# Kernel optimization log

Measured on AMD Instinct MI355X. Metric: run time of the kernel, lower is better.

## Reference

```python
import jax, jax.numpy as jnp
import numpy as np

H = 3  # hidden size (matches nn.LSTM(3, 3, ...))


def _lstm_dir(x, Wih, Whh, bih, bhh, reverse):
    """One direction of one LSTM layer. x: [B,T,D]; PyTorch gate order i,f,g,o."""
    B = x.shape[0]
    xT = jnp.swapaxes(x, 0, 1)  # [T,B,D]
    # Precompute input projection for all timesteps (memory-bound GEMM once).
    x_proj = jnp.einsum('tbd,gd->tbg', xT, Wih) + (bih + bhh)  # [T,B,4H]

    def step(carry, xp):
        h, c = carry
        gates = xp + h @ Whh.T  # [B,4H]
        i = jax.nn.sigmoid(gates[:, :H])
        f = jax.nn.sigmoid(gates[:, H:2 * H])
        g = jnp.tanh(gates[:, 2 * H:3 * H])
        o = jax.nn.sigmoid(gates[:, 3 * H:])
        c = f * c + i * g
        h = o * jnp.tanh(c)
        return (h, c), h

    init = (jnp.zeros((B, H), x.dtype), jnp.zeros((B, H), x.dtype))
    _, hs = jax.lax.scan(step, init, x_proj, reverse=reverse)
    return jnp.swapaxes(hs, 0, 1)  # [B,T,H], time-aligned with input


def setup_inputs() -> dict:
    key = jax.random.key(0)
    ks = jax.random.split(key, 20)
    B, T = 8192, 512
    k = 1.0 / np.sqrt(H)

    def u(kk, shape):
        return jax.random.uniform(kk, shape, jnp.float32, -k, k)

    inp = {"x": jax.random.normal(ks[0], (B, T, 3), jnp.float32)}
    # layer 0: input dim 3; layer 1: input dim 2*H = 6
    inp.update({
        "W_ih_l0": u(ks[1], (4 * H, 3)),  "W_hh_l0": u(ks[2], (4 * H, H)),
        "b_ih_l0": u(ks[3], (4 * H,)),    "b_hh_l0": u(ks[4], (4 * H,)),
        "W_ih_l0r": u(ks[5], (4 * H, 3)), "W_hh_l0r": u(ks[6], (4 * H, H)),
        "b_ih_l0r": u(ks[7], (4 * H,)),   "b_hh_l0r": u(ks[8], (4 * H,)),
        "W_ih_l1": u(ks[9], (4 * H, 2 * H)),  "W_hh_l1": u(ks[10], (4 * H, H)),
        "b_ih_l1": u(ks[11], (4 * H,)),       "b_hh_l1": u(ks[12], (4 * H,)),
        "W_ih_l1r": u(ks[13], (4 * H, 2 * H)),"W_hh_l1r": u(ks[14], (4 * H, H)),
        "b_ih_l1r": u(ks[15], (4 * H,)),      "b_hh_l1r": u(ks[16], (4 * H,)),
        "W_lin": u(ks[17], (1, 2 * H)),       "b_lin": u(ks[18], (1,)),
    })
    return inp


def reference(x, W_ih_l0, W_hh_l0, b_ih_l0, b_hh_l0,
              W_ih_l0r, W_hh_l0r, b_ih_l0r, b_hh_l0r,
              W_ih_l1, W_hh_l1, b_ih_l1, b_hh_l1,
              W_ih_l1r, W_hh_l1r, b_ih_l1r, b_hh_l1r,
              W_lin, b_lin):
    # layer 0 (bidirectional)
    y0 = jnp.concatenate([
        _lstm_dir(x, W_ih_l0, W_hh_l0, b_ih_l0, b_hh_l0, False),
        _lstm_dir(x, W_ih_l0r, W_hh_l0r, b_ih_l0r, b_hh_l0r, True),
    ], axis=-1)  # [B,T,6]
    # layer 1 (bidirectional)
    y1 = jnp.concatenate([
        _lstm_dir(y0, W_ih_l1, W_hh_l1, b_ih_l1, b_hh_l1, False),
        _lstm_dir(y0, W_ih_l1r, W_hh_l1r, b_ih_l1r, b_hh_l1r, True),
    ], axis=-1)  # [B,T,6]
    last = y1[:, -1, :]  # [B,6]  (output sequence at final timestep)
    out = last @ W_lin.T + b_lin  # [B,1]
    return jax.nn.sigmoid(out.reshape(-1))  # [B]
```

## Files before the change

kernel.cpp:

```cpp
#include <hip/hip_runtime.h>


#define B_ 8192
#define T_ 512
#define LOG2E 1.4426950408889634f

typedef float v2f __attribute__((ext_vector_type(2)));

__device__ __forceinline__ float rcp_(float x)  { return __builtin_amdgcn_rcpf(x); }
__device__ __forceinline__ float exp2_(float x) { return __builtin_amdgcn_exp2f(x); }
__device__ __forceinline__ float sigm_(float x) {
  return rcp_(1.0f + exp2_(-LOG2E * x));
}
__device__ __forceinline__ float tanh_(float x) {
  return 1.0f - 2.0f * rcp_(1.0f + exp2_(2.0f * LOG2E * x));
}
__device__ __forceinline__ float act_(float p) { return rcp_(1.f + exp2_(p)); }

__device__ __forceinline__ v2f sp(float s) { return (v2f){s, s}; }
__device__ __forceinline__ v2f pkfma(v2f a, float b, v2f c) {
  return __builtin_elementwise_fma(a, sp(b), c);
}

template <int CTRL>
__device__ __forceinline__ float dppf(float v) {
  int s = __float_as_int(v);
  return __int_as_float(__builtin_amdgcn_update_dpp(s, s, CTRL, 0xF, 0xF, false));
}
#define QP0 dppf<0x00>
#define QP1 dppf<0x55>
#define QP2 dppf<0xAA>
#define QP3 dppf<0xFF>
#define SHL4 0x104
#define SHR4 0x114


template <bool DIRB>
__device__ __forceinline__ void l0_run(
    const float* __restrict__ x,
    const float* __restrict__ Wi, const float* __restrict__ Wh,
    const float* __restrict__ bi, const float* __restrict__ bh,
    float* __restrict__ yout, int b, int jl)
{
  const int jj = (jl < 3) ? jl : 0;
  const int ri = jj, rf = 3 + jj, rg = 6 + jj, ro = 9 + jj;
  const float sL = -LOG2E, sG = -2.f * LOG2E;

  float wi_i0 = Wi[ri*3+0]*sL, wi_i1 = Wi[ri*3+1]*sL, wi_i2 = Wi[ri*3+2]*sL;
  float wi_f0 = Wi[rf*3+0]*sL, wi_f1 = Wi[rf*3+1]*sL, wi_f2 = Wi[rf*3+2]*sL;
  float wi_g0 = Wi[rg*3+0]*sG, wi_g1 = Wi[rg*3+1]*sG, wi_g2 = Wi[rg*3+2]*sG;
  float wi_o0 = Wi[ro*3+0]*sL, wi_o1 = Wi[ro*3+1]*sL, wi_o2 = Wi[ro*3+2]*sL;
  float wh_i0 = Wh[ri*3+0]*sL, wh_i1 = Wh[ri*3+1]*sL, wh_i2 = Wh[ri*3+2]*sL;
  float wh_f0 = Wh[rf*3+0]*sL, wh_f1 = Wh[rf*3+1]*sL, wh_f2 = Wh[rf*3+2]*sL;
  float wh_g0 = Wh[rg*3+0]*sG, wh_g1 = Wh[rg*3+1]*sG, wh_g2 = Wh[rg*3+2]*sG;
  float wh_o0 = Wh[ro*3+0]*sL, wh_o1 = Wh[ro*3+1]*sL, wh_o2 = Wh[ro*3+2]*sL;
  float b_i = (bi[ri]+bh[ri])*sL, b_f = (bi[rf]+bh[rf])*sL;
  float b_g = (bi[rg]+bh[rg])*sG, b_o = (bi[ro]+bh[ro])*sL;

  float h = 0.f, c = 0.f, ha0 = 0.f, ha1 = 0.f, ha2 = 0.f;
  float hs0, hs1, hs2, hs3, hs4, hs5, hs6, hs7;

  const float*  xrow = x + (size_t)b * (T_ * 3);
  const float4* xq4  = (const float4*)xrow;
  const float2* xq2  = (const float2*)(xrow);
  float* ybase = yout + (size_t)b * (T_ * 3) + jj * 8;

  float4 pA; float2 pB; float4 qA; float2 qB;

#define LDQ(blk, A_, B_) do {                                             \
    A_ = xq4[(blk) * 6 + jl];                                             \
    B_ = xq2[(blk) * 12 + 8 + jl];                                        \
    __builtin_amdgcn_sched_barrier(0); } while (0)

#define STEPS(X0, X1, X2, HOUT) do {                                      \
    float _x0 = (X0), _x1 = (X1), _x2 = (X2);                             \
    float _pi = __builtin_fmaf(wi_i0, _x0, b_i);                          \
    _pi = __builtin_fmaf(wi_i1, _x1, _pi);                                \
    _pi = __builtin_fmaf(wi_i2, _x2, _pi);                                \
    float _qi = wh_i0 * ha0;                                              \
    _qi = __builtin_fmaf(wh_i1, ha1, _qi);                                \
    _qi = __builtin_fmaf(wh_i2, ha2, _qi);                                \
    float _pf = __builtin_fmaf(wi_f0, _x0, b_f);                          \
    _pf = __builtin_fmaf(wi_f1, _x1, _pf);                                \
    _pf = __builtin_fmaf(wi_f2, _x2, _pf);                                \
    float _qf = wh_f0 * ha0;                                              \
    _qf = __builtin_fmaf(wh_f1, ha1, _qf);                                \
    _qf = __builtin_fmaf(wh_f2, ha2, _qf);                                \
    float _pg = __builtin_fmaf(wi_g0, _x0, b_g);                          \
    _pg = __builtin_fmaf(wi_g1, _x1, _pg);                                \
    _pg = __builtin_fmaf(wi_g2, _x2, _pg);                                \
    float _qg = wh_g0 * ha0;                                              \
    _qg = __builtin_fmaf(wh_g1, ha1, _qg);                                \
    _qg = __builtin_fmaf(wh_g2, ha2, _qg);                                \
    float _po = __builtin_fmaf(wi_o0, _x0, b_o);                          \
    _po = __builtin_fmaf(wi_o1, _x1, _po);                                \
    _po = __builtin_fmaf(wi_o2, _x2, _po);                                \
    float _qo = wh_o0 * ha0;                                              \
    _qo = __builtin_fmaf(wh_o1, ha1, _qo);                                \
    _qo = __builtin_fmaf(wh_o2, ha2, _qo);                                \
    float _ig = act_(_pi + _qi);                                          \
    float _fg = act_(_pf + _qf);                                          \
    float _gg = __builtin_fmaf(2.f, act_(_pg + _qg), -1.f);               \
    float _og = act_(_po + _qo);                                          \
    c = __builtin_fmaf(_fg, c, _ig * _gg);                                \
    float _th = __builtin_fmaf(                                           \
        2.f, rcp_(1.f + exp2_(-2.f * LOG2E * c)), -1.f);                  \
    h = _og * _th;                                                        \
    ha0 = QP0(h); ha1 = QP1(h); ha2 = QP2(h);                             \
    HOUT = h; } while (0)

#define S0(A_, B_) STEPS(QP0(A_.x), QP0(A_.y), QP0(A_.z), hs0)
#define S1(A_, B_) STEPS(QP0(A_.w), QP1(A_.x), QP1(A_.y), hs1)
#define S2(A_, B_) STEPS(QP1(A_.z), QP1(A_.w), QP2(A_.x), hs2)
#define S3(A_, B_) STEPS(QP2(A_.y), QP2(A_.z), QP2(A_.w), hs3)
#define S4(A_, B_) STEPS(QP3(A_.x), QP3(A_.y), QP3(A_.z), hs4)
#define S5(A_, B_) STEPS(QP3(A_.w), QP0(B_.x), QP0(B_.y), hs5)
#define S6(A_, B_) STEPS(QP1(B_.x), QP1(B_.y), QP2(B_.x), hs6)
#define S7(A_, B_) STEPS(QP2(B_.y), QP3(B_.x), QP3(B_.y), hs7)

#define PROCQ(A_, B_) do {                                                \
    if (DIRB) { S7(A_,B_); S6(A_,B_); S5(A_,B_); S4(A_,B_);               \
                S3(A_,B_); S2(A_,B_); S1(A_,B_); S0(A_,B_); }             \
    else      { S0(A_,B_); S1(A_,B_); S2(A_,B_); S3(A_,B_);               \
                S4(A_,B_); S5(A_,B_); S6(A_,B_); S7(A_,B_); } } while (0)

#define STQ(blk) do {                                                     \
    if (jl < 3) {                                                         \
      float4* _o = (float4*)(ybase + (blk) * 24);                         \
      _o[0] = make_float4(hs0, hs1, hs2, hs3);                            \
      _o[1] = make_float4(hs4, hs5, hs6, hs7);                            \
    } } while (0)

#define BLK(k) (DIRB ? (63 - (k)) : (k))

  LDQ(BLK(0), pA, pB);
  LDQ(BLK(1), qA, qB);
  for (int k = 0; k < 64; k += 2) {
    PROCQ(pA, pB);
    STQ(BLK(k));
    if (k + 2 < 64) LDQ(BLK(k + 2), pA, pB);
    PROCQ(qA, qB);
    STQ(BLK(k + 1));
    if (k + 3 < 64) LDQ(BLK(k + 3), qA, qB);
  }
#undef LDQ
#undef STEPS
#undef S0
#undef S1
#undef S2
#undef S3
#undef S4
#undef S5
#undef S6
#undef S7
#undef PROCQ
#undef STQ
#undef BLK
}

__global__ __launch_bounds__(256, 2) void lstm_l0_scalar(
    const float* __restrict__ x,
    const float* __restrict__ Wf_ih, const float* __restrict__ Wf_hh,
    const float* __restrict__ bf_ih, const float* __restrict__ bf_hh,
    const float* __restrict__ Wr_ih, const float* __restrict__ Wr_hh,
    const float* __restrict__ br_ih, const float* __restrict__ br_hh,
    float* __restrict__ y0f, float* __restrict__ y0b)
{
  int gid = blockIdx.x * 256 + threadIdx.x;
  const int nfwd = B_ * 4;
  if (gid < nfwd) {
    int b = gid >> 2, jl = gid & 3;
    l0_run<false>(x, Wf_ih, Wf_hh, bf_ih, bf_hh, y0f, b, jl);
  } else {
    int g2 = gid - nfwd;
    int b = g2 >> 2, jl = g2 & 3;
    l0_run<true>(x, Wr_ih, Wr_hh, br_ih, br_hh, y0b, b, jl);
  }
}

#define CELL_TAIL(HOUT)                                                   \
    float r0v = act_(pv.x);                                               \
    float ayv = act_(pv.y);                                               \
    float axv = __builtin_fmaf(avx, r0v, dvx);                            \
    float slx = dppf<SHL4>(axv), sly = dppf<SHL4>(ayv);                   \
    float srx = dppf<SHR4>(axv), sry = dppf<SHR4>(ayv);                   \
    float pig = axv * (qgo ? srx : slx);                                  \
    float gf  = qgo ? sry : ayv;                                          \
    float gO  = qgo ? ayv : sly;                                          \
    c = __builtin_fmaf(gf, c, pig);                                       \
    float th = __builtin_fmaf(                                            \
        2.f, rcp_(1.f + exp2_(-2.f * LOG2E * c)), -1.f);                  \
    h = gO * th;                                                          \
    ha0 = QP0(h); ha1 = QP1(h); ha2 = QP2(h);                             \
    HOUT = h;

__global__ __launch_bounds__(256, 1) void lstm_l1_fwd(
    const float* __restrict__ Wih1, const float* __restrict__ Whh1,
    const float* __restrict__ bih1, const float* __restrict__ bhh1,
    const float* __restrict__ Wih1r,
    const float* __restrict__ bih1r, const float* __restrict__ bhh1r,
    const float* __restrict__ Wlin, const float* __restrict__ blin,
    const float* __restrict__ y0f, const float* __restrict__ y0b,
    float* __restrict__ out)
{
  int tid  = blockIdx.x * 256 + threadIdx.x;
  int b    = tid >> 3;
  int lane = tid & 7;
  bool qgo = (lane & 4) != 0;
  int j = lane & 3; int jj = (j < 3) ? j : 0;
  const int ra = (qgo ? 6 : 0) + jj, rb = ra + 3;
  const float kx = qgo ? (-2.f * LOG2E) : (-LOG2E);
  const float ky = -LOG2E;
  const float avx = qgo ? 2.f : 1.f;
  const float dvx = qgo ? -1.f : 0.f;

  v2f w0 = {Wih1[ra*6+0]*kx, Wih1[rb*6+0]*ky},
      w1 = {Wih1[ra*6+1]*kx, Wih1[rb*6+1]*ky},
      w2 = {Wih1[ra*6+2]*kx, Wih1[rb*6+2]*ky},
      w3 = {Wih1[ra*6+3]*kx, Wih1[rb*6+3]*ky},
      w4 = {Wih1[ra*6+4]*kx, Wih1[rb*6+4]*ky},
      w5 = {Wih1[ra*6+5]*kx, Wih1[rb*6+5]*ky};
  v2f u0 = {Whh1[ra*3+0]*kx, Whh1[rb*3+0]*ky},
      u1 = {Whh1[ra*3+1]*kx, Whh1[rb*3+1]*ky},
      u2 = {Whh1[ra*3+2]*kx, Whh1[rb*3+2]*ky};
  v2f b2 = {(bih1[ra]+bhh1[ra])*kx, (bih1[rb]+bhh1[rb])*ky};

  const float4* yfq = (const float4*)(y0f + (size_t)b * (T_ * 3));
  const float4* ybq = (const float4*)(y0b + (size_t)b * (T_ * 3));

  const float* ufp = y0f + (size_t)b * (T_ * 3) + 63 * 24 + 7;
  const float* ubp = y0b + (size_t)b * (T_ * 3) + 63 * 24 + 7;
  float uf0 = ufp[0], uf1 = ufp[8], uf2 = ufp[16];
  float ub0 = ubp[0], ub1 = ubp[8], ub2 = ubp[16];

  float h = 0.f, c = 0.f, ha0 = 0.f, ha1 = 0.f, ha2 = 0.f;
  float hs0, hs1, hs2, hs3, hs4, hs5, hs6, hs7;
  float4 pf0, pf1, pf2, pf3, pf4, pf5, pb0, pb1, pb2, pb3, pb4, pb5;
  float4 qf0, qf1, qf2, qf3, qf4, qf5, qb0, qb1, qb2, qb3, qb4, qb5;

#define LDB(blk, F0,F1,F2,F3,F4,F5, G0,G1,G2,G3,G4,G5) do {               \
    const float4* _f = yfq + (blk) * 6;                                   \
    const float4* _g = ybq + (blk) * 6;                                   \
    F0 = _f[0]; F1 = _f[1]; F2 = _f[2];                                   \
    F3 = _f[3]; F4 = _f[4]; F5 = _f[5];                                   \
    G0 = _g[0]; G1 = _g[1]; G2 = _g[2];                                   \
    G3 = _g[3]; G4 = _g[4]; G5 = _g[5];                                   \
    __builtin_amdgcn_sched_barrier(0); } while (0)

#define STEPB(f0, f1, f2, g0, g1, g2, HOUT) do {                          \
    v2f pv = pkfma(w0, (f0), b2); pv = pkfma(w1, (f1), pv);               \
    pv = pkfma(w2, (f2), pv);                                             \
    v2f nv = w3 * sp(g0); nv = pkfma(w4, (g1), nv);                       \
    nv = pkfma(w5, (g2), nv);                                             \
    v2f uv = u0 * sp(ha0); uv = pkfma(u1, ha1, uv);                       \
    uv = pkfma(u2, ha2, uv);                                              \
    pv = (pv + nv) + uv;                                                  \
    CELL_TAIL(HOUT) } while (0)

#define PROCB(F0,F1,F2,F3,F4,F5, G0,G1,G2,G3,G4,G5) do {                  \
    STEPB(F0.x, F2.x, F4.x,  G0.x, G2.x, G4.x, hs0);                      \
    STEPB(F0.y, F2.y, F4.y,  G0.y, G2.y, G4.y, hs1);                      \
    STEPB(F0.z, F2.z, F4.z,  G0.z, G2.z, G4.z, hs2);                      \
    STEPB(F0.w, F2.w, F4.w,  G0.w, G2.w, G4.w, hs3);                      \
    STEPB(F1.x, F3.x, F5.x,  G1.x, G3.x, G5.x, hs4);                      \
    STEPB(F1.y, F3.y, F5.y,  G1.y, G3.y, G5.y, hs5);                      \
    STEPB(F1.z, F3.z, F5.z,  G1.z, G3.z, G5.z, hs6);                      \
    STEPB(F1.w, F3.w, F5.w,  G1.w, G3.w, G5.w, hs7); } while (0)

  LDB(0, pf0,pf1,pf2,pf3,pf4,pf5, pb0,pb1,pb2,pb3,pb4,pb5);
  LDB(1, qf0,qf1,qf2,qf3,qf4,qf5, qb0,qb1,qb2,qb3,qb4,qb5);
  for (int it = 0; it < 32; ++it) {
    PROCB(pf0,pf1,pf2,pf3,pf4,pf5, pb0,pb1,pb2,pb3,pb4,pb5);
    if (it < 31) LDB(2*it+2, pf0,pf1,pf2,pf3,pf4,pf5, pb0,pb1,pb2,pb3,pb4,pb5);
    PROCB(qf0,qf1,qf2,qf3,qf4,qf5, qb0,qb1,qb2,qb3,qb4,qb5);
    if (it < 31) LDB(2*it+3, qf0,qf1,qf2,qf3,qf4,qf5, qb0,qb1,qb2,qb3,qb4,qb5);
  }
  (void)hs0; (void)hs1; (void)hs2; (void)hs3;
  (void)hs4; (void)hs5; (void)hs6; (void)hs7;

  float h1b;
  {
    v2f r0 = {Wih1r[ra*6+0]*kx, Wih1r[rb*6+0]*ky},
        r1 = {Wih1r[ra*6+1]*kx, Wih1r[rb*6+1]*ky},
        r2 = {Wih1r[ra*6+2]*kx, Wih1r[rb*6+2]*ky},
        r3 = {Wih1r[ra*6+3]*kx, Wih1r[rb*6+3]*ky},
        r4 = {Wih1r[ra*6+4]*kx, Wih1r[rb*6+4]*ky},
        r5 = {Wih1r[ra*6+5]*kx, Wih1r[rb*6+5]*ky};
    v2f br = {(bih1r[ra]+bhh1r[ra])*kx, (bih1r[rb]+bhh1r[rb])*ky};
    v2f qv = pkfma(r0, uf0, br); qv = pkfma(r1, uf1, qv);
    qv = pkfma(r2, uf2, qv);     qv = pkfma(r3, ub0, qv);
    qv = pkfma(r4, ub1, qv);     qv = pkfma(r5, ub2, qv);
    float r0v = act_(qv.x);
    float ayv = act_(qv.y);
    float axv = __builtin_fmaf(avx, r0v, dvx);
    float slx = dppf<SHL4>(axv), sly = dppf<SHL4>(ayv);
    float srx = dppf<SHR4>(axv);
    float gi = qgo ? srx : axv;
    float gG = qgo ? axv : slx;
    float gO = qgo ? ayv : sly;
    float cb = gi * gG;
    h1b = gO * tanh_(cb);
  }

  float part = 0.f;
  if (!qgo && j < 3) part = __builtin_fmaf(Wlin[j], h, Wlin[3 + j] * h1b);
  part += __shfl_xor(part, 1, 8);
  part += __shfl_xor(part, 2, 8);
  part += __shfl_xor(part, 4, 8);
  if (lane == 0) out[b] = sigm_(part + blin[0]);
#undef LDB
#undef STEPB
#undef PROCB
}

extern "C" void kernel_launch(void* const* d_in, const int* in_sizes, int n_in,
                              void* d_out, int out_size, void* d_ws, size_t ws_size,
                              hipStream_t stream) {
  const float* x        = (const float*)d_in[0];
  const float* W_ih_l0  = (const float*)d_in[1];
  const float* W_hh_l0  = (const float*)d_in[2];
  const float* b_ih_l0  = (const float*)d_in[3];
  const float* b_hh_l0  = (const float*)d_in[4];
  const float* W_ih_l0r = (const float*)d_in[5];
  const float* W_hh_l0r = (const float*)d_in[6];
  const float* b_ih_l0r = (const float*)d_in[7];
  const float* b_hh_l0r = (const float*)d_in[8];
  const float* W_ih_l1  = (const float*)d_in[9];
  const float* W_hh_l1  = (const float*)d_in[10];
  const float* b_ih_l1  = (const float*)d_in[11];
  const float* b_hh_l1  = (const float*)d_in[12];
  const float* W_ih_l1r = (const float*)d_in[13];
  const float* b_ih_l1r = (const float*)d_in[15];
  const float* b_hh_l1r = (const float*)d_in[16];
  const float* W_lin    = (const float*)d_in[17];
  const float* b_lin    = (const float*)d_in[18];

  float* y0f = (float*)d_ws;
  float* y0b = (float*)d_ws + (size_t)B_ * T_ * 3;
  float* out = (float*)d_out;

  lstm_l0_scalar<<<(B_ * 4 * 2) / 256, 256, 0, stream>>>(
      x, W_ih_l0, W_hh_l0, b_ih_l0, b_hh_l0,
      W_ih_l0r, W_hh_l0r, b_ih_l0r, b_hh_l0r, y0f, y0b);

  lstm_l1_fwd<<<(B_ * 8) / 256, 256, 0, stream>>>(
      W_ih_l1, W_hh_l1, b_ih_l1, b_hh_l1,
      W_ih_l1r, b_ih_l1r, b_hh_l1r,
      W_lin, b_lin, y0f, y0b, out);
}
```

Measured before the change: 151.9 us.

## Load full x blocks per lane, pin weights in VGPRs, relax launch bounds

Layer 0 no longer loads a per-lane float4+float2 slice and redistributes x across the quad with DPP. Each lane now loads all six float4s of a 24-element block directly, which removes the DPP broadcasts from the recurrence path but multiplies load traffic and register use. Empty asm constraints pin the weights and biases in VGPRs so the compiler cannot rematerialize or spill them. The launch_bounds min-blocks hints are dropped, and the layer-1 tail loads are moved after the loop to shorten their live range.

```diff
diff --git a/kernel.cpp b/kernel.cpp
--- a/kernel.cpp
+++ b/kernel.cpp
@@ -22,6 +22,12 @@
   return __builtin_elementwise_fma(a, sp(b), c);
 }
 
+#define PIN1(v) asm volatile("" : "+v"(v))
+#define PIN2(v) do {                                                      \
+    double _d = __builtin_bit_cast(double, v);                            \
+    asm volatile("" : "+v"(_d));                                          \
+    v = __builtin_bit_cast(v2f, _d); } while (0)
+
 template <int CTRL>
 __device__ __forceinline__ float dppf(float v) {
   int s = __float_as_int(v);
@@ -30,10 +36,8 @@
 #define QP0 dppf<0x00>
 #define QP1 dppf<0x55>
 #define QP2 dppf<0xAA>
-#define QP3 dppf<0xFF>
 #define SHL4 0x104
 #define SHR4 0x114
-
 
 template <bool DIRB>
 __device__ __forceinline__ void l0_run(
@@ -57,19 +61,28 @@
   float b_i = (bi[ri]+bh[ri])*sL, b_f = (bi[rf]+bh[rf])*sL;
   float b_g = (bi[rg]+bh[rg])*sG, b_o = (bi[ro]+bh[ro])*sL;
 
+  PIN1(wi_i0); PIN1(wi_i1); PIN1(wi_i2);
+  PIN1(wi_f0); PIN1(wi_f1); PIN1(wi_f2);
+  PIN1(wi_g0); PIN1(wi_g1); PIN1(wi_g2);
+  PIN1(wi_o0); PIN1(wi_o1); PIN1(wi_o2);
+  PIN1(wh_i0); PIN1(wh_i1); PIN1(wh_i2);
+  PIN1(wh_f0); PIN1(wh_f1); PIN1(wh_f2);
+  PIN1(wh_g0); PIN1(wh_g1); PIN1(wh_g2);
+  PIN1(wh_o0); PIN1(wh_o1); PIN1(wh_o2);
+  PIN1(b_i); PIN1(b_f); PIN1(b_g); PIN1(b_o);
+
   float h = 0.f, c = 0.f, ha0 = 0.f, ha1 = 0.f, ha2 = 0.f;
   float hs0, hs1, hs2, hs3, hs4, hs5, hs6, hs7;
 
-  const float*  xrow = x + (size_t)b * (T_ * 3);
-  const float4* xq4  = (const float4*)xrow;
-  const float2* xq2  = (const float2*)(xrow);
+  const float4* xq4 = (const float4*)(x + (size_t)b * (T_ * 3));
   float* ybase = yout + (size_t)b * (T_ * 3) + jj * 8;
 
-  float4 pA; float2 pB; float4 qA; float2 qB;
-
-#define LDQ(blk, A_, B_) do {                                             \
-    A_ = xq4[(blk) * 6 + jl];                                             \
-    B_ = xq2[(blk) * 12 + 8 + jl];                                        \
+  float4 p0, p1, p2, p3, p4, p5, q0, q1, q2, q3, q4, q5;
+
+#define LDQ(blk, R0, R1, R2, R3, R4, R5) do {                             \
+    const float4* _p = xq4 + (blk) * 6;                                   \
+    R0 = _p[0]; R1 = _p[1]; R2 = _p[2];                                   \
+    R3 = _p[3]; R4 = _p[4]; R5 = _p[5];                                   \
     __builtin_amdgcn_sched_barrier(0); } while (0)
 
 #define STEPS(X0, X1, X2, HOUT) do {                                      \
@@ -109,20 +122,27 @@
     ha0 = QP0(h); ha1 = QP1(h); ha2 = QP2(h);                             \
     HOUT = h; } while (0)
 
-#define S0(A_, B_) STEPS(QP0(A_.x), QP0(A_.y), QP0(A_.z), hs0)
-#define S1(A_, B_) STEPS(QP0(A_.w), QP1(A_.x), QP1(A_.y), hs1)
-#define S2(A_, B_) STEPS(QP1(A_.z), QP1(A_.w), QP2(A_.x), hs2)
-#define S3(A_, B_) STEPS(QP2(A_.y), QP2(A_.z), QP2(A_.w), hs3)
-#define S4(A_, B_) STEPS(QP3(A_.x), QP3(A_.y), QP3(A_.z), hs4)
-#define S5(A_, B_) STEPS(QP3(A_.w), QP0(B_.x), QP0(B_.y), hs5)
-#define S6(A_, B_) STEPS(QP1(B_.x), QP1(B_.y), QP2(B_.x), hs6)
-#define S7(A_, B_) STEPS(QP2(B_.y), QP3(B_.x), QP3(B_.y), hs7)
-
-#define PROCQ(A_, B_) do {                                                \
-    if (DIRB) { S7(A_,B_); S6(A_,B_); S5(A_,B_); S4(A_,B_);               \
-                S3(A_,B_); S2(A_,B_); S1(A_,B_); S0(A_,B_); }             \
-    else      { S0(A_,B_); S1(A_,B_); S2(A_,B_); S3(A_,B_);               \
-                S4(A_,B_); S5(A_,B_); S6(A_,B_); S7(A_,B_); } } while (0)
+#define S0(R0,R1,R2,R3,R4,R5) STEPS(R0.x, R0.y, R0.z, hs0)
+#define S1(R0,R1,R2,R3,R4,R5) STEPS(R0.w, R1.x, R1.y, hs1)
+#define S2(R0,R1,R2,R3,R4,R5) STEPS(R1.z, R1.w, R2.x, hs2)
+#define S3(R0,R1,R2,R3,R4,R5) STEPS(R2.y, R2.z, R2.w, hs3)
+#define S4(R0,R1,R2,R3,R4,R5) STEPS(R3.x, R3.y, R3.z, hs4)
+#define S5(R0,R1,R2,R3,R4,R5) STEPS(R3.w, R4.x, R4.y, hs5)
+#define S6(R0,R1,R2,R3,R4,R5) STEPS(R4.z, R4.w, R5.x, hs6)
+#define S7(R0,R1,R2,R3,R4,R5) STEPS(R5.y, R5.z, R5.w, hs7)
+
+#define PROCQ(R0,R1,R2,R3,R4,R5) do {                                     \
+    if (DIRB) {                                                           \
+      S7(R0,R1,R2,R3,R4,R5); S6(R0,R1,R2,R3,R4,R5);                       \
+      S5(R0,R1,R2,R3,R4,R5); S4(R0,R1,R2,R3,R4,R5);                       \
+      S3(R0,R1,R2,R3,R4,R5); S2(R0,R1,R2,R3,R4,R5);                       \
+      S1(R0,R1,R2,R3,R4,R5); S0(R0,R1,R2,R3,R4,R5);                       \
+    } else {                                                              \
+      S0(R0,R1,R2,R3,R4,R5); S1(R0,R1,R2,R3,R4,R5);                       \
+      S2(R0,R1,R2,R3,R4,R5); S3(R0,R1,R2,R3,R4,R5);                       \
+      S4(R0,R1,R2,R3,R4,R5); S5(R0,R1,R2,R3,R4,R5);                       \
+      S6(R0,R1,R2,R3,R4,R5); S7(R0,R1,R2,R3,R4,R5);                       \
+    } } while (0)
 
 #define STQ(blk) do {                                                     \
     if (jl < 3) {                                                         \
@@ -133,15 +153,15 @@
 
 #define BLK(k) (DIRB ? (63 - (k)) : (k))
 
-  LDQ(BLK(0), pA, pB);
-  LDQ(BLK(1), qA, qB);
+  LDQ(BLK(0), p0, p1, p2, p3, p4, p5);
+  LDQ(BLK(1), q0, q1, q2, q3, q4, q5);
   for (int k = 0; k < 64; k += 2) {
-    PROCQ(pA, pB);
+    PROCQ(p0, p1, p2, p3, p4, p5);
     STQ(BLK(k));
-    if (k + 2 < 64) LDQ(BLK(k + 2), pA, pB);
-    PROCQ(qA, qB);
+    if (k + 2 < 64) LDQ(BLK(k + 2), p0, p1, p2, p3, p4, p5);
+    PROCQ(q0, q1, q2, q3, q4, q5);
     STQ(BLK(k + 1));
-    if (k + 3 < 64) LDQ(BLK(k + 3), qA, qB);
+    if (k + 3 < 64) LDQ(BLK(k + 3), q0, q1, q2, q3, q4, q5);
   }
 #undef LDQ
 #undef STEPS
@@ -158,7 +178,7 @@
 #undef BLK
 }
 
-__global__ __launch_bounds__(256, 2) void lstm_l0_scalar(
+__global__ __launch_bounds__(256) void lstm_l0_scalar(
     const float* __restrict__ x,
     const float* __restrict__ Wf_ih, const float* __restrict__ Wf_hh,
     const float* __restrict__ bf_ih, const float* __restrict__ bf_hh,
@@ -194,7 +214,7 @@
     ha0 = QP0(h); ha1 = QP1(h); ha2 = QP2(h);                             \
     HOUT = h;
 
-__global__ __launch_bounds__(256, 1) void lstm_l1_fwd(
+__global__ __launch_bounds__(256) void lstm_l1_fwd(
     const float* __restrict__ Wih1, const float* __restrict__ Whh1,
     const float* __restrict__ bih1, const float* __restrict__ bhh1,
     const float* __restrict__ Wih1r,
@@ -224,14 +244,14 @@
       u1 = {Whh1[ra*3+1]*kx, Whh1[rb*3+1]*ky},
       u2 = {Whh1[ra*3+2]*kx, Whh1[rb*3+2]*ky};
   v2f b2 = {(bih1[ra]+bhh1[ra])*kx, (bih1[rb]+bhh1[rb])*ky};
+  PIN2(w0); PIN2(w1); PIN2(w2); PIN2(w3); PIN2(w4); PIN2(w5);
+  PIN2(u0); PIN2(u1); PIN2(u2); PIN2(b2);
 
   const float4* yfq = (const float4*)(y0f + (size_t)b * (T_ * 3));
   const float4* ybq = (const float4*)(y0b + (size_t)b * (T_ * 3));
 
   const float* ufp = y0f + (size_t)b * (T_ * 3) + 63 * 24 + 7;
   const float* ubp = y0b + (size_t)b * (T_ * 3) + 63 * 24 + 7;
-  float uf0 = ufp[0], uf1 = ufp[8], uf2 = ufp[16];
-  float ub0 = ubp[0], ub1 = ubp[8], ub2 = ubp[16];
 
   float h = 0.f, c = 0.f, ha0 = 0.f, ha1 = 0.f, ha2 = 0.f;
   float hs0, hs1, hs2, hs3, hs4, hs5, hs6, hs7;
@@ -277,6 +297,9 @@
   }
   (void)hs0; (void)hs1; (void)hs2; (void)hs3;
   (void)hs4; (void)hs5; (void)hs6; (void)hs7;
+
+  float uf0 = ufp[0], uf1 = ufp[8], uf2 = ufp[16];
+  float ub0 = ubp[0], ub1 = ubp[8], ub2 = ubp[16];
 
   float h1b;
   {
```

New measurement: 145.9 us. 1.04x faster.
